# Kernel optimization log

Measured on AMD Instinct MI355X. Metric: run time of the kernel, lower is better.

Reference implementation:

```python
import jax, jax.numpy as jnp
import numpy as np

B, T, D, H, OUT_STEPS = 4096, 50, 64, 128, 100  # batch, warmup steps, latent dim, hidden units, rollout steps


def setup_inputs() -> dict:
    key = jax.random.key(0)
    ks = jax.random.split(key, 9)
    s = jnp.float32(0.05)  # keep gates out of saturation
    return {
        "x":   jax.random.normal(ks[0], (B, T, D), jnp.float32),
        "Wk0": jax.random.normal(ks[1], (D, 4 * H), jnp.float32) * s,
        "Wr0": jax.random.normal(ks[2], (H, 4 * H), jnp.float32) * s,
        "b0":  jax.random.normal(ks[3], (4 * H,), jnp.float32) * s,
        "Wk1": jax.random.normal(ks[4], (H, 4 * H), jnp.float32) * s,
        "Wr1": jax.random.normal(ks[5], (H, 4 * H), jnp.float32) * s,
        "b1":  jax.random.normal(ks[6], (4 * H,), jnp.float32) * s,
        "Wd":  jax.random.normal(ks[7], (H, D), jnp.float32) * s,
        "bd":  jax.random.normal(ks[8], (D,), jnp.float32) * s,
    }


def _lstm_cell(xt, h, c, Wk, Wr, b):
    # Keras LSTMCell: gates in order i, f, g(cell), o
    z = xt @ Wk + h @ Wr + b  # [B, 4H]
    i, f, g, o = jnp.split(z, 4, axis=-1)
    c_new = jax.nn.sigmoid(f) * c + jax.nn.sigmoid(i) * jnp.tanh(g)
    h_new = jax.nn.sigmoid(o) * jnp.tanh(c_new)
    return h_new, c_new


def reference(x, Wk0, Wr0, b0, Wk1, Wr1, b1, Wd, bd):
    Bn = x.shape[0]
    Hn = Wr0.shape[0]
    z = jnp.zeros((Bn, Hn), x.dtype)

    def warm_step(carry, xt):
        h0, c0, h1, c1 = carry
        h0, c0 = _lstm_cell(xt, h0, c0, Wk0, Wr0, b0)
        h1, c1 = _lstm_cell(h0, h1, c1, Wk1, Wr1, b1)
        return (h0, c0, h1, c1), None

    # warmup over the provided sequence (T >= min_warmup_steps=10)
    carry, _ = jax.lax.scan(warm_step, (z, z, z, z), jnp.swapaxes(x, 0, 1))
    pred0 = carry[2] @ Wd + bd  # Dense on last layer's hidden state

    def ar_step(carry, _):
        pred, h0, c0, h1, c1 = carry
        h0, c0 = _lstm_cell(pred, h0, c0, Wk0, Wr0, b0)
        h1, c1 = _lstm_cell(h0, h1, c1, Wk1, Wr1, b1)
        pred = h1 @ Wd + bd
        return (pred, h0, c0, h1, c1), pred

    _, preds = jax.lax.scan(ar_step, (pred0,) + carry, None, length=OUT_STEPS - 1)
    preds = jnp.concatenate([pred0[None], preds], axis=0)  # [OUT, B, D]
    return jnp.swapaxes(preds, 0, 1)  # [B, OUT, D]
```

## Files before the change

### kernel.cpp

```cpp
#include <hip/hip_runtime.h>
#include <hip/hip_bf16.h>

#define Tt   50
#define Dd   64
#define NOUT 100
#define G4   512
#define K0P  200
#define K1P  264
#define BM   16

typedef __attribute__((ext_vector_type(8))) short  short8;
typedef __attribute__((ext_vector_type(4))) float  floatx4;

__device__ __forceinline__ float fsig(float v)  { return __builtin_amdgcn_rcpf(1.0f + __expf(-v)); }
__device__ __forceinline__ float ftanh_(float v) { return 2.0f * __builtin_amdgcn_rcpf(1.0f + __expf(-2.0f * v)) - 1.0f; }
__device__ __forceinline__ short f2bf(float f) {
    __hip_bfloat16 h = __float2bfloat16(f);
    return *reinterpret_cast<const short*>(&h);
}

#define W1F_OFF 196608
#define WDF_OFF 458752
#define B0F_OFF 475136
#define B1F_OFF 477184
#define BDF_OFF 479232

__global__ __launch_bounds__(256) void prep_kernel(
    const float* __restrict__ Wk0, const float* __restrict__ Wr0, const float* __restrict__ b0,
    const float* __restrict__ Wk1, const float* __restrict__ Wr1, const float* __restrict__ b1,
    const float* __restrict__ Wd,  const float* __restrict__ bd,  char* __restrict__ ws)
{
    int idx = blockIdx.x * 256 + threadIdx.x;
    short* w0f = (short*)ws;
    short* w1f = (short*)(ws + W1F_OFF);
    short* wdf = (short*)(ws + WDF_OFF);
    float* b0f = (float*)(ws + B0F_OFF);
    float* b1f = (float*)(ws + B1F_OFF);
    float* bdf = (float*)(ws + BDF_OFF);

    if (idx < 98304) {
        int f = idx >> 9, r = idx & 511;
        int lane = r >> 3, j = r & 7;
        int nt = f / 6, kt = f - nt * 6;
        int k = kt * 32 + (lane >> 4) * 8 + j;
        int col = nt * 16 + (lane & 15);
        w0f[idx] = f2bf((k < Dd) ? Wk0[k * G4 + col] : Wr0[(k - Dd) * G4 + col]);
    } else if (idx < 229376) {
        int i2 = idx - 98304;
        int f = i2 >> 9, r = i2 & 511;
        int lane = r >> 3, j = r & 7;
        int nt = f >> 3, kt = f & 7;
        int k = kt * 32 + (lane >> 4) * 8 + j;
        int col = nt * 16 + (lane & 15);
        w1f[i2] = f2bf((k < 128) ? Wk1[k * G4 + col] : Wr1[(k - 128) * G4 + col]);
    } else if (idx < 237568) {
        int i2 = idx - 229376;
        int f = i2 >> 9, r = i2 & 511;
        int lane = r >> 3, j = r & 7;
        int nt = f >> 2, kt = f & 3;
        int k = kt * 32 + (lane >> 4) * 8 + j;
        int col = nt * 16 + (lane & 15);
        wdf[i2] = f2bf(Wd[k * Dd + col]);
    } else if (idx < 237568 + 1088) {
        int i2 = idx - 237568;
        if (i2 < 512)       b0f[i2]        = b0[i2];
        else if (i2 < 1024) b1f[i2 - 512]  = b1[i2 - 512];
        else                bdf[i2 - 1024] = bd[i2 - 1024];
    }
}

#define SM_A1  6400
#define SM_WD  14848
#define SM_W0  31232
#define SM_TOT 162304

__global__ __launch_bounds__(512, 2) void lstm_kernel(
    const float* __restrict__ x, const char* __restrict__ ws, float* __restrict__ out)
{
    extern __shared__ char smem[];
    short* a0  = (short*)smem;
    short* a1  = (short*)(smem + SM_A1);
    short* wdl = (short*)(smem + SM_WD);
    short* w0l = (short*)(smem + SM_W0);

    const short* w0f = (const short*)ws;
    const short* w1f = (const short*)(ws + W1F_OFF);
    const short* wdf = (const short*)(ws + WDF_OFF);
    const float* b0f = (const float*)(ws + B0F_OFF);
    const float* b1f = (const float*)(ws + B1F_OFF);
    const float* bdf = (const float*)(ws + BDF_OFF);

    const int tid  = threadIdx.x;
    const int w    = tid >> 6;
    const int lane = tid & 63;
    const int l15  = lane & 15;
    const int quad = lane >> 4;
    const int row0 = blockIdx.x * BM;

    for (int i = tid; i < BM * K0P; i += 512) a0[i] = 0;
    for (int i = tid; i < BM * K1P; i += 512) a1[i] = 0;
    for (int i = tid; i < 8192; i += 512) wdl[i] = wdf[i];
    for (int c = tid; c < 8192; c += 512) {
        int e8 = c & 63;
        int wv = (c >> 6) & 7;
        int p  = c >> 9;
        int g = p / 6, kt = p - g * 6;
        const short* src = w0f + ((((g * 8 + wv) * 6) + kt) << 9) + e8 * 8;
        *(short8*)&w0l[((p * 8 + wv) << 9) + e8 * 8] = *(const short8*)src;
    }

    const short* w0b = w0f + w * 3072 + lane * 8;
    const short* w1b = w1f + w * 4096 + lane * 8;
    short8 W1R[4][8];
    #pragma unroll
    for (int g = 0; g < 4; ++g)
        #pragma unroll
        for (int kt = 0; kt < 8; ++kt)
            W1R[g][kt] = *(const short8*)(w1b + g * 32768 + kt * 512);
    short8 W0R[8];
    #pragma unroll
    for (int p = 16; p < 24; ++p) {
        int g = p / 6, kt = p - g * 6;
        W0R[p - 16] = *(const short8*)(w0b + g * 24576 + kt * 512);
    }

    const int hu = w * 16 + l15;
    const float bi0 = b0f[hu], bff0 = b0f[128 + hu], bg0 = b0f[256 + hu], bo0 = b0f[384 + hu];
    const float bi1 = b1f[hu], bff1 = b1f[128 + hu], bg1 = b1f[256 + hu], bo1 = b1f[384 + hu];
    const float bdv = bdf[(w & 3) * 16 + l15];

    float c0s[4] = {0.f, 0.f, 0.f, 0.f};
    float c1s[4] = {0.f, 0.f, 0.f, 0.f};

    __syncthreads();

    for (int step = 0; step < 149; ++step) {
        if (step < Tt) {
            int colx = tid & 63, rg = tid >> 6;
            #pragma unroll
            for (int kk = 0; kk < 2; ++kk) {
                int r = rg + 8 * kk;
                a0[r * K0P + colx] = f2bf(x[(size_t)(row0 + r) * (Tt * Dd) + step * Dd + colx]);
            }
        }
        __syncthreads();

        floatx4 acc[4];
        #pragma unroll
        for (int g = 0; g < 4; ++g) acc[g] = (floatx4){0.f, 0.f, 0.f, 0.f};

        #pragma unroll
        for (int kt = 0; kt < 6; ++kt) {
            short8 af = *(const short8*)&a0[l15 * K0P + kt * 32 + quad * 8];
            #pragma unroll
            for (int g = 0; g < 4; ++g) {
                int p = g * 6 + kt;
                short8 bfr = (p < 16) ? *(const short8*)&w0l[((p * 8 + w) << 9) + lane * 8]
                                      : W0R[p - 16];
                acc[g] = __builtin_amdgcn_mfma_f32_16x16x32_bf16(af, bfr, acc[g], 0, 0, 0);
            }
        }
        __syncthreads();

        #pragma unroll
        for (int r = 0; r < 4; ++r) {
            float zi = acc[0][r] + bi0;
            float zf = acc[1][r] + bff0;
            float zg = acc[2][r] + bg0;
            float zo = acc[3][r] + bo0;
            float c  = fsig(zf) * c0s[r] + fsig(zi) * ftanh_(zg);
            c0s[r] = c;
            float h  = fsig(zo) * ftanh_(c);
            short hb = f2bf(h);
            int row = quad * 4 + r;
            a0[row * K0P + 64 + hu] = hb;
            a1[row * K1P + hu]      = hb;
        }
        __syncthreads();

        #pragma unroll
        for (int g = 0; g < 4; ++g) acc[g] = (floatx4){0.f, 0.f, 0.f, 0.f};

        #pragma unroll
        for (int kt = 0; kt < 8; ++kt) {
            short8 af = *(const short8*)&a1[l15 * K1P + kt * 32 + quad * 8];
            #pragma unroll
            for (int g = 0; g < 4; ++g)
                acc[g] = __builtin_amdgcn_mfma_f32_16x16x32_bf16(af, W1R[g][kt], acc[g], 0, 0, 0);
        }
        __syncthreads();

        #pragma unroll
        for (int r = 0; r < 4; ++r) {
            float zi = acc[0][r] + bi1;
            float zf = acc[1][r] + bff1;
            float zg = acc[2][r] + bg1;
            float zo = acc[3][r] + bo1;
            float c  = fsig(zf) * c1s[r] + fsig(zi) * ftanh_(zg);
            c1s[r] = c;
            float h  = fsig(zo) * ftanh_(c);
            int row = quad * 4 + r;
            a1[row * K1P + 128 + hu] = f2bf(h);
        }

        if (step >= Tt - 1) {
            __syncthreads();
            if (w < 4) {
                floatx4 ad = (floatx4){0.f, 0.f, 0.f, 0.f};
                #pragma unroll
                for (int kt = 0; kt < 4; ++kt) {
                    short8 a_ = *(const short8*)&a1[l15 * K1P + 128 + kt * 32 + quad * 8];
                    short8 b_ = *(const short8*)&wdl[((w * 4 + kt) << 9) + lane * 8];
                    ad = __builtin_amdgcn_mfma_f32_16x16x32_bf16(a_, b_, ad, 0, 0, 0);
                }
                int s = step - (Tt - 1);
                #pragma unroll
                for (int r = 0; r < 4; ++r) {
                    float p = ad[r] + bdv;
                    int row = quad * 4 + r;
                    int col = w * 16 + l15;
                    out[(size_t)(row0 + row) * (NOUT * Dd) + s * Dd + col] = p;
                    a0[row * K0P + col] = f2bf(p);
                }
            }
        }
    }
}

extern "C" void kernel_launch(void* const* d_in, const int* in_sizes, int n_in,
                              void* d_out, int out_size, void* d_ws, size_t ws_size,
                              hipStream_t stream)
{
    (void)in_sizes; (void)n_in; (void)out_size; (void)ws_size;
    static_assert(SM_TOT <= 160 * 1024, "LDS budget");
    hipFuncSetAttribute(reinterpret_cast<const void*>(lstm_kernel),
                        hipFuncAttributeMaxDynamicSharedMemorySize, SM_TOT);
    prep_kernel<<<933, 256, 0, stream>>>(
        (const float*)d_in[1], (const float*)d_in[2], (const float*)d_in[3],
        (const float*)d_in[4], (const float*)d_in[5], (const float*)d_in[6],
        (const float*)d_in[7], (const float*)d_in[8], (char*)d_ws);
    lstm_kernel<<<256, 512, SM_TOT, stream>>>(
        (const float*)d_in[0], (const char*)d_ws, (float*)d_out);
}
```

Measured before the change: 542.8 us.

## Double-buffer LSTM activations to cut barriers, fold exp scaling and bias into weights

Activation buffers in LDS are now double-buffered by step parity. This removes two of the four per-step barriers, and layer 0 reads h0 from the previous layer-1 input buffer instead of keeping a separate copy. The next x timestep is prefetched into registers before the matmul. Gate weights and biases are prescaled by -log2(e) (or -2·log2(e) for the tanh gate) so the activations use exp2 directly. Biases initialize the accumulators, and the dense weights move from LDS into registers. The changes add register pressure under the 2-waves-per-SIMD launch bound, and the extra bf16 rounding of the prescaled weights may shift numerics slightly.

```diff
diff --git a/kernel.cpp b/kernel.cpp
--- a/kernel.cpp
+++ b/kernel.cpp
@@ -5,15 +5,23 @@
 #define Dd   64
 #define NOUT 100
 #define G4   512
-#define K0P  200
+#define K0S  72
 #define K1P  264
 #define BM   16
 
 typedef __attribute__((ext_vector_type(8))) short  short8;
 typedef __attribute__((ext_vector_type(4))) float  floatx4;
 
-__device__ __forceinline__ float fsig(float v)  { return __builtin_amdgcn_rcpf(1.0f + __expf(-v)); }
-__device__ __forceinline__ float ftanh_(float v) { return 2.0f * __builtin_amdgcn_rcpf(1.0f + __expf(-2.0f * v)) - 1.0f; }
+#if __has_builtin(__builtin_amdgcn_exp2f)
+#define EXP2(v) __builtin_amdgcn_exp2f(v)
+#else
+#define EXP2(v) exp2f(v)
+#endif
+__device__ __forceinline__ float rcp_(float v) { return __builtin_amdgcn_rcpf(v); }
+__device__ __forceinline__ float fsig2(float u)  { return rcp_(1.0f + EXP2(u)); }
+__device__ __forceinline__ float ftanh2(float u) { return fmaf(2.0f, rcp_(1.0f + EXP2(u)), -1.0f); }
+#define KN2L2E (-2.8853900817779268f)
+
 __device__ __forceinline__ short f2bf(float f) {
     __hip_bfloat16 h = __float2bfloat16(f);
     return *reinterpret_cast<const short*>(&h);
@@ -37,6 +45,8 @@
     float* b0f = (float*)(ws + B0F_OFF);
     float* b1f = (float*)(ws + B1F_OFF);
     float* bdf = (float*)(ws + BDF_OFF);
+    const float NL2E = -1.4426950408889634f;
+    const float N2L2E = -2.8853900817779268f;
 
     if (idx < 98304) {
         int f = idx >> 9, r = idx & 511;
@@ -44,7 +54,8 @@
         int nt = f / 6, kt = f - nt * 6;
         int k = kt * 32 + (lane >> 4) * 8 + j;
         int col = nt * 16 + (lane & 15);
-        w0f[idx] = f2bf((k < Dd) ? Wk0[k * G4 + col] : Wr0[(k - Dd) * G4 + col]);
+        float sc = ((col >> 7) == 2) ? N2L2E : NL2E;
+        w0f[idx] = f2bf(sc * ((k < Dd) ? Wk0[k * G4 + col] : Wr0[(k - Dd) * G4 + col]));
     } else if (idx < 229376) {
         int i2 = idx - 98304;
         int f = i2 >> 9, r = i2 & 511;
@@ -52,7 +63,8 @@
         int nt = f >> 3, kt = f & 7;
         int k = kt * 32 + (lane >> 4) * 8 + j;
         int col = nt * 16 + (lane & 15);
-        w1f[i2] = f2bf((k < 128) ? Wk1[k * G4 + col] : Wr1[(k - 128) * G4 + col]);
+        float sc = ((col >> 7) == 2) ? N2L2E : NL2E;
+        w1f[i2] = f2bf(sc * ((k < 128) ? Wk1[k * G4 + col] : Wr1[(k - 128) * G4 + col]));
     } else if (idx < 237568) {
         int i2 = idx - 229376;
         int f = i2 >> 9, r = i2 & 511;
@@ -63,24 +75,29 @@
         wdf[i2] = f2bf(Wd[k * Dd + col]);
     } else if (idx < 237568 + 1088) {
         int i2 = idx - 237568;
-        if (i2 < 512)       b0f[i2]        = b0[i2];
-        else if (i2 < 1024) b1f[i2 - 512]  = b1[i2 - 512];
-        else                bdf[i2 - 1024] = bd[i2 - 1024];
-    }
-}
-
-#define SM_A1  6400
-#define SM_WD  14848
-#define SM_W0  31232
-#define SM_TOT 162304
+        if (i2 < 512) {
+            float sc = ((i2 >> 7) == 2) ? N2L2E : NL2E;
+            b0f[i2] = sc * b0[i2];
+        } else if (i2 < 1024) {
+            int c = i2 - 512;
+            float sc = ((c >> 7) == 2) ? N2L2E : NL2E;
+            b1f[c] = sc * b1[c];
+        } else bdf[i2 - 1024] = bd[i2 - 1024];
+    }
+}
+
+#define SM_A1  4608
+#define SM_W0  21504
+#define SM_TOT 152576
+#define A0SZ   1152
+#define A1SZ   4224
 
 __global__ __launch_bounds__(512, 2) void lstm_kernel(
     const float* __restrict__ x, const char* __restrict__ ws, float* __restrict__ out)
 {
     extern __shared__ char smem[];
-    short* a0  = (short*)smem;
-    short* a1  = (short*)(smem + SM_A1);
-    short* wdl = (short*)(smem + SM_WD);
+    short* a0b = (short*)smem;
+    short* a1b = (short*)(smem + SM_A1);
     short* w0l = (short*)(smem + SM_W0);
 
     const short* w0f = (const short*)ws;
@@ -97,9 +114,8 @@
     const int quad = lane >> 4;
     const int row0 = blockIdx.x * BM;
 
-    for (int i = tid; i < BM * K0P; i += 512) a0[i] = 0;
-    for (int i = tid; i < BM * K1P; i += 512) a1[i] = 0;
-    for (int i = tid; i < 8192; i += 512) wdl[i] = wdf[i];
+    for (int i = tid; i < 2 * A0SZ; i += 512) a0b[i] = 0;
+    for (int i = tid; i < 2 * A1SZ; i += 512) a1b[i] = 0;
     for (int c = tid; c < 8192; c += 512) {
         int e8 = c & 63;
         int wv = (c >> 6) & 7;
@@ -108,20 +124,31 @@
         const short* src = w0f + ((((g * 8 + wv) * 6) + kt) << 9) + e8 * 8;
         *(short8*)&w0l[((p * 8 + wv) << 9) + e8 * 8] = *(const short8*)src;
     }
-
-    const short* w0b = w0f + w * 3072 + lane * 8;
-    const short* w1b = w1f + w * 4096 + lane * 8;
+    {
+        int colx = tid & 63, rg = tid >> 6;
+        a0b[rg * K0S + colx]       = f2bf(x[(size_t)(row0 + rg) * (Tt * Dd) + colx]);
+        a0b[(rg + 8) * K0S + colx] = f2bf(x[(size_t)(row0 + rg + 8) * (Tt * Dd) + colx]);
+    }
+
+    const short* w0rb = w0f + w * 3072 + lane * 8;
+    const short* w1rb = w1f + w * 4096 + lane * 8;
     short8 W1R[4][8];
     #pragma unroll
     for (int g = 0; g < 4; ++g)
         #pragma unroll
         for (int kt = 0; kt < 8; ++kt)
-            W1R[g][kt] = *(const short8*)(w1b + g * 32768 + kt * 512);
+            W1R[g][kt] = *(const short8*)(w1rb + g * 32768 + kt * 512);
     short8 W0R[8];
     #pragma unroll
     for (int p = 16; p < 24; ++p) {
         int g = p / 6, kt = p - g * 6;
-        W0R[p - 16] = *(const short8*)(w0b + g * 24576 + kt * 512);
+        W0R[p - 16] = *(const short8*)(w0rb + g * 24576 + kt * 512);
+    }
+    short8 WdR[4];
+    if (w < 4) {
+        #pragma unroll
+        for (int kt = 0; kt < 4; ++kt)
+            WdR[kt] = *(const short8*)(wdf + ((w * 4 + kt) << 9) + lane * 8);
     }
 
     const int hu = w * 16 + l15;
@@ -132,97 +159,104 @@
     float c0s[4] = {0.f, 0.f, 0.f, 0.f};
     float c1s[4] = {0.f, 0.f, 0.f, 0.f};
 
+    const int colx = tid & 63, rg = tid >> 6;
+
     __syncthreads();
 
     for (int step = 0; step < 149; ++step) {
-        if (step < Tt) {
-            int colx = tid & 63, rg = tid >> 6;
-            #pragma unroll
-            for (int kk = 0; kk < 2; ++kk) {
-                int r = rg + 8 * kk;
-                a0[r * K0P + colx] = f2bf(x[(size_t)(row0 + r) * (Tt * Dd) + step * Dd + colx]);
-            }
-        }
-        __syncthreads();
+        const int p = step & 1, q = p ^ 1;
+        short* a0p = a0b + p * A0SZ;  short* a0q = a0b + q * A0SZ;
+        short* a1p = a1b + p * A1SZ;  short* a1q = a1b + q * A1SZ;
+
+        float xv0, xv1;
+        if (step < Tt - 1) {
+            xv0 = x[(size_t)(row0 + rg)     * (Tt * Dd) + (step + 1) * Dd + colx];
+            xv1 = x[(size_t)(row0 + rg + 8) * (Tt * Dd) + (step + 1) * Dd + colx];
+        }
 
         floatx4 acc[4];
-        #pragma unroll
-        for (int g = 0; g < 4; ++g) acc[g] = (floatx4){0.f, 0.f, 0.f, 0.f};
+        acc[0] = (floatx4){bi0,  bi0,  bi0,  bi0};
+        acc[1] = (floatx4){bff0, bff0, bff0, bff0};
+        acc[2] = (floatx4){bg0,  bg0,  bg0,  bg0};
+        acc[3] = (floatx4){bo0,  bo0,  bo0,  bo0};
 
         #pragma unroll
         for (int kt = 0; kt < 6; ++kt) {
-            short8 af = *(const short8*)&a0[l15 * K0P + kt * 32 + quad * 8];
+            short8 af = (kt < 2)
+                ? *(const short8*)&a0p[l15 * K0S + kt * 32 + quad * 8]
+                : *(const short8*)&a1q[l15 * K1P + (kt - 2) * 32 + quad * 8];
             #pragma unroll
             for (int g = 0; g < 4; ++g) {
-                int p = g * 6 + kt;
-                short8 bfr = (p < 16) ? *(const short8*)&w0l[((p * 8 + w) << 9) + lane * 8]
-                                      : W0R[p - 16];
+                int pp = g * 6 + kt;
+                short8 bfr = (pp < 16) ? *(const short8*)&w0l[((pp * 8 + w) << 9) + lane * 8]
+                                       : W0R[pp - 16];
                 acc[g] = __builtin_amdgcn_mfma_f32_16x16x32_bf16(af, bfr, acc[g], 0, 0, 0);
             }
         }
+
+        #pragma unroll
+        for (int r = 0; r < 4; ++r) {
+            float si = fsig2(acc[0][r]);
+            float sf = fsig2(acc[1][r]);
+            float tg = ftanh2(acc[2][r]);
+            float so = fsig2(acc[3][r]);
+            float c  = fmaf(sf, c0s[r], si * tg);
+            c0s[r] = c;
+            float h  = so * ftanh2(c * KN2L2E);
+            a1p[(quad * 4 + r) * K1P + hu] = f2bf(h);
+        }
+
+        if (step < Tt - 1) {
+            a0q[rg * K0S + colx]       = f2bf(xv0);
+            a0q[(rg + 8) * K0S + colx] = f2bf(xv1);
+        }
         __syncthreads();
 
-        #pragma unroll
-        for (int r = 0; r < 4; ++r) {
-            float zi = acc[0][r] + bi0;
-            float zf = acc[1][r] + bff0;
-            float zg = acc[2][r] + bg0;
-            float zo = acc[3][r] + bo0;
-            float c  = fsig(zf) * c0s[r] + fsig(zi) * ftanh_(zg);
-            c0s[r] = c;
-            float h  = fsig(zo) * ftanh_(c);
-            short hb = f2bf(h);
-            int row = quad * 4 + r;
-            a0[row * K0P + 64 + hu] = hb;
-            a1[row * K1P + hu]      = hb;
-        }
-        __syncthreads();
-
-        #pragma unroll
-        for (int g = 0; g < 4; ++g) acc[g] = (floatx4){0.f, 0.f, 0.f, 0.f};
+        acc[0] = (floatx4){bi1,  bi1,  bi1,  bi1};
+        acc[1] = (floatx4){bff1, bff1, bff1, bff1};
+        acc[2] = (floatx4){bg1,  bg1,  bg1,  bg1};
+        acc[3] = (floatx4){bo1,  bo1,  bo1,  bo1};
 
         #pragma unroll
         for (int kt = 0; kt < 8; ++kt) {
-            short8 af = *(const short8*)&a1[l15 * K1P + kt * 32 + quad * 8];
+            short8 af = *(const short8*)&a1p[l15 * K1P + kt * 32 + quad * 8];
             #pragma unroll
             for (int g = 0; g < 4; ++g)
                 acc[g] = __builtin_amdgcn_mfma_f32_16x16x32_bf16(af, W1R[g][kt], acc[g], 0, 0, 0);
         }
-        __syncthreads();
 
         #pragma unroll
         for (int r = 0; r < 4; ++r) {
-            float zi = acc[0][r] + bi1;
-            float zf = acc[1][r] + bff1;
-            float zg = acc[2][r] + bg1;
-            float zo = acc[3][r] + bo1;
-            float c  = fsig(zf) * c1s[r] + fsig(zi) * ftanh_(zg);
+            float si = fsig2(acc[0][r]);
+            float sf = fsig2(acc[1][r]);
+            float tg = ftanh2(acc[2][r]);
+            float so = fsig2(acc[3][r]);
+            float c  = fmaf(sf, c1s[r], si * tg);
             c1s[r] = c;
-            float h  = fsig(zo) * ftanh_(c);
-            int row = quad * 4 + r;
-            a1[row * K1P + 128 + hu] = f2bf(h);
+            float h  = so * ftanh2(c * KN2L2E);
+            a1q[(quad * 4 + r) * K1P + 128 + hu] = f2bf(h);
         }
 
         if (step >= Tt - 1) {
             __syncthreads();
             if (w < 4) {
-                floatx4 ad = (floatx4){0.f, 0.f, 0.f, 0.f};
+                floatx4 ad = (floatx4){bdv, bdv, bdv, bdv};
                 #pragma unroll
                 for (int kt = 0; kt < 4; ++kt) {
-                    short8 a_ = *(const short8*)&a1[l15 * K1P + 128 + kt * 32 + quad * 8];
-                    short8 b_ = *(const short8*)&wdl[((w * 4 + kt) << 9) + lane * 8];
-                    ad = __builtin_amdgcn_mfma_f32_16x16x32_bf16(a_, b_, ad, 0, 0, 0);
+                    short8 a_ = *(const short8*)&a1q[l15 * K1P + 128 + kt * 32 + quad * 8];
+                    ad = __builtin_amdgcn_mfma_f32_16x16x32_bf16(a_, WdR[kt], ad, 0, 0, 0);
                 }
                 int s = step - (Tt - 1);
                 #pragma unroll
                 for (int r = 0; r < 4; ++r) {
-                    float p = ad[r] + bdv;
+                    float pv = ad[r];
                     int row = quad * 4 + r;
                     int col = w * 16 + l15;
-                    out[(size_t)(row0 + row) * (NOUT * Dd) + s * Dd + col] = p;
-                    a0[row * K0P + col] = f2bf(p);
+                    out[(size_t)(row0 + row) * (NOUT * Dd) + s * Dd + col] = pv;
+                    a0q[row * K0S + col] = f2bf(pv);
                 }
             }
+            __syncthreads();
         }
     }
 }
```

New measurement: 505.9 us. 1.07x faster.
